# Kernel tuning notes

Hardware: AMD Instinct MI355X
Metric: run time of the kernel (lower is better)

The kernel has to match this reference:

```python
import jax, jax.numpy as jnp
import numpy as np
import math

B, T, C = 2, 2048, 1024
N_HEADS = 16  # config.head_size in the original (actually number of heads)
HEAD_DIM = C // N_HEADS


def setup_inputs() -> dict:
    key = jax.random.key(0)
    k1, k2, k3 = jax.random.split(key, 3)
    s = 1.0 / math.sqrt(C)
    return {
        "x": jax.random.normal(k1, (B, T, C), dtype=jnp.float32),
        "W_attn": jax.random.normal(k2, (C, 3 * C), dtype=jnp.float32) * s,
        "b_attn": jnp.zeros((3 * C,), dtype=jnp.float32),
        "W_proj": jax.random.normal(k3, (C, C), dtype=jnp.float32) * s,
        "b_proj": jnp.zeros((C,), dtype=jnp.float32),
    }


def reference(x, W_attn, b_attn, W_proj, b_proj):
    Bsz, Tlen, Cdim = x.shape
    qkv = x @ W_attn + b_attn                      # [B,T,3C]
    q, k, v = jnp.split(qkv, 3, axis=-1)
    # [B,T,C] -> [B,H,T,D]
    def to_heads(t):
        return t.reshape(Bsz, Tlen, N_HEADS, HEAD_DIM).transpose(0, 2, 1, 3)
    q, k, v = to_heads(q), to_heads(k), to_heads(v)
    # NOTE: original multiplies by sqrt(head_dim) (faithful to source, not 1/sqrt)
    scale = jnp.asarray(math.sqrt(HEAD_DIM), dtype=x.dtype)
    att = jnp.einsum("bhqd,bhkd->bhqk", q, k) * scale
    causal = jnp.tril(jnp.ones((Tlen, Tlen), dtype=bool))
    att = jnp.where(causal[None, None, :, :], att, jnp.asarray(-jnp.inf, x.dtype))
    att = jax.nn.softmax(att, axis=-1)
    # dropout layers are identity in eval mode
    y = jnp.einsum("bhqk,bhkd->bhqd", att, v)
    y = y.transpose(0, 2, 1, 3).reshape(Bsz, Tlen, Cdim)
    return y @ W_proj + b_proj
```

## Files before the change

kernel.cpp:

```cpp
#include <hip/hip_runtime.h>
#include <hip/hip_bf16.h>


#define B_  2
#define T_  2048
#define C_  1024
#define H_  16
#define D_  64
#define M_  (B_ * T_)
#define N3_ (3 * C_)

typedef __attribute__((ext_vector_type(8))) short s16x8;
typedef __attribute__((ext_vector_type(4))) short s16x4;
typedef __attribute__((ext_vector_type(4))) float f32x4;

typedef const __attribute__((address_space(1))) unsigned int gu32_t;
typedef __attribute__((address_space(3))) unsigned int lu32_t;

__device__ __forceinline__ void gload_lds16(const short* g, short* l) {
    __builtin_amdgcn_global_load_lds((gu32_t*)g, (lu32_t*)l, 16, 0, 0);
}

__device__ __forceinline__ float b2f(unsigned short u) {
    return __uint_as_float(((unsigned)u) << 16);
}
__device__ __forceinline__ unsigned short f2b(float f) {
    unsigned u = __float_as_uint(f);
    return (unsigned short)((u + 0x7FFFu + ((u >> 16) & 1u)) >> 16);
}
__device__ __forceinline__ float fexp2(float x) {
#if __has_builtin(__builtin_amdgcn_exp2f)
    return __builtin_amdgcn_exp2f(x);
#else
    return exp2f(x);
#endif
}

__global__ __launch_bounds__(256) void cvt_split(
    const float* __restrict__ in, short* __restrict__ oh, short* __restrict__ ol, int n)
{
    int i = (blockIdx.x * 256 + threadIdx.x) * 8;
    if (i >= n) return;
    float4 a = *(const float4*)&in[i];
    float4 b = *(const float4*)&in[i + 4];
    float v[8] = {a.x, a.y, a.z, a.w, b.x, b.y, b.z, b.w};
    s16x8 h, l;
    #pragma unroll
    for (int j = 0; j < 8; j++) {
        unsigned short hb = f2b(v[j]);
        h[j] = (short)hb;
        l[j] = (short)f2b(v[j] - b2f(hb));
    }
    *(s16x8*)&oh[i] = h;
    *(s16x8*)&ol[i] = l;
}

__global__ __launch_bounds__(256) void cvtT_split(
    const float* __restrict__ in, short* __restrict__ oh, short* __restrict__ ol,
    int R, int Cn)
{
    __shared__ short th[64][80];
    __shared__ short tl[64][80];
    const int tid = threadIdx.x;
    const int k0 = blockIdx.y * 64;
    const int n0 = blockIdx.x * 64;
    {
        int rl = tid >> 4, cl = (tid & 15) * 4;
        #pragma unroll
        for (int i = 0; i < 4; i++) {
            int kr = rl + i * 16;
            float4 v4 = *(const float4*)&in[(size_t)(k0 + kr) * Cn + n0 + cl];
            float v[4] = {v4.x, v4.y, v4.z, v4.w};
            #pragma unroll
            for (int j = 0; j < 4; j++) {
                unsigned short hb = f2b(v[j]);
                th[cl + j][kr] = (short)hb;
                tl[cl + j][kr] = (short)f2b(v[j] - b2f(hb));
            }
        }
    }
    __syncthreads();
    {
        int ro = tid >> 2, co = (tid & 3) * 16;
        *(s16x8*)&oh[(size_t)(n0 + ro) * R + k0 + co]     = *(s16x8*)&th[ro][co];
        *(s16x8*)&oh[(size_t)(n0 + ro) * R + k0 + co + 8] = *(s16x8*)&th[ro][co + 8];
        *(s16x8*)&ol[(size_t)(n0 + ro) * R + k0 + co]     = *(s16x8*)&tl[ro][co];
        *(s16x8*)&ol[(size_t)(n0 + ro) * R + k0 + co + 8] = *(s16x8*)&tl[ro][co + 8];
    }
}

__global__ __launch_bounds__(256) void cvtT_bf16(
    const float* __restrict__ in, short* __restrict__ out, int R, int Cn)
{
    __shared__ short t[64][80];
    const int tid = threadIdx.x;
    const int k0 = blockIdx.y * 64;
    const int n0 = blockIdx.x * 64;
    {
        int rl = tid >> 4, cl = (tid & 15) * 4;
        #pragma unroll
        for (int i = 0; i < 4; i++) {
            int kr = rl + i * 16;
            float4 v = *(const float4*)&in[(size_t)(k0 + kr) * Cn + n0 + cl];
            t[cl + 0][kr] = (short)f2b(v.x);
            t[cl + 1][kr] = (short)f2b(v.y);
            t[cl + 2][kr] = (short)f2b(v.z);
            t[cl + 3][kr] = (short)f2b(v.w);
        }
    }
    __syncthreads();
    {
        int ro = tid >> 2, co = (tid & 3) * 16;
        *(s16x8*)&out[(size_t)(n0 + ro) * R + k0 + co]     = *(s16x8*)&t[ro][co];
        *(s16x8*)&out[(size_t)(n0 + ro) * R + k0 + co + 8] = *(s16x8*)&t[ro][co + 8];
    }
}

__global__ __launch_bounds__(256) void qkv_qk(
    const short* __restrict__ Ah, const short* __restrict__ Al,
    const short* __restrict__ BTh, const short* __restrict__ BTl,
    const float* __restrict__ bias,
    short* __restrict__ Qh, short* __restrict__ Ql,
    short* __restrict__ Kh, short* __restrict__ Kl)
{
    __shared__ short Ash[128 * 32], Asl[128 * 32];
    __shared__ short Bsh[128 * 32], Bsl[128 * 32];

    const int tid  = threadIdx.x;
    const int wave = tid >> 6, lane = tid & 63;
    const int wm = wave >> 1, wn = wave & 1;
    const int lm = lane & 15, lq = lane >> 4;
    const int m0 = blockIdx.y * 128, n0 = blockIdx.x * 128;
    const int gr = (lane >> 2);
    const int gc = (lane & 3) * 8;

    f32x4 acc[4][4] = {};

    for (int k0 = 0; k0 < C_; k0 += 32) {
        __syncthreads();
        #pragma unroll
        for (int j = 0; j < 2; j++) {
            int s = wave * 2 + j;
            int row = s * 16 + gr;
            size_t ga = (size_t)(m0 + row) * C_ + k0 + gc;
            size_t gb = (size_t)(n0 + row) * C_ + k0 + gc;
            gload_lds16(&Ah[ga],  &Ash[s * 512]);
            gload_lds16(&Al[ga],  &Asl[s * 512]);
            gload_lds16(&BTh[gb], &Bsh[s * 512]);
            gload_lds16(&BTl[gb], &Bsl[s * 512]);
        }
        __syncthreads();

        s16x8 ah[4], al[4], bh[4], bl[4];
        #pragma unroll
        for (int mi = 0; mi < 4; mi++) {
            int r = wm * 64 + mi * 16 + lm;
            ah[mi] = *(const s16x8*)&Ash[r * 32 + lq * 8];
            al[mi] = *(const s16x8*)&Asl[r * 32 + lq * 8];
        }
        #pragma unroll
        for (int nj = 0; nj < 4; nj++) {
            int r = wn * 64 + nj * 16 + lm;
            bh[nj] = *(const s16x8*)&Bsh[r * 32 + lq * 8];
            bl[nj] = *(const s16x8*)&Bsl[r * 32 + lq * 8];
        }
        #pragma unroll
        for (int mi = 0; mi < 4; mi++)
            #pragma unroll
            for (int nj = 0; nj < 4; nj++) {
                acc[mi][nj] = __builtin_amdgcn_mfma_f32_16x16x32_bf16(
                    ah[mi], bh[nj], acc[mi][nj], 0, 0, 0);
                acc[mi][nj] = __builtin_amdgcn_mfma_f32_16x16x32_bf16(
                    ah[mi], bl[nj], acc[mi][nj], 0, 0, 0);
                acc[mi][nj] = __builtin_amdgcn_mfma_f32_16x16x32_bf16(
                    al[mi], bh[nj], acc[mi][nj], 0, 0, 0);
            }
    }

    #pragma unroll
    for (int nj = 0; nj < 4; nj++) {
        int n = n0 + wn * 64 + nj * 16 + lm;
        float bv = bias[n];
        int isK = n >> 10;
        int c = n & (C_ - 1);
        int h = c >> 6, d = c & (D_ - 1);
        short* dh = isK ? Kh : Qh;
        short* dl = isK ? Kl : Ql;
        float scale = isK ? 1.0f : 11.541560327111708f;
        #pragma unroll
        for (int mi = 0; mi < 4; mi++) {
            #pragma unroll
            for (int r = 0; r < 4; r++) {
                int m  = m0 + wm * 64 + mi * 16 + lq * 4 + r;
                int bb = m >> 11, t = m & (T_ - 1);
                float v = (acc[mi][nj][r] + bv) * scale;
                size_t idx = (((size_t)bb * H_ + h) * T_ + t) * D_ + d;
                unsigned short hb = f2b(v);
                dh[idx] = (short)hb;
                dl[idx] = (short)f2b(v - b2f(hb));
            }
        }
    }
}

__global__ __launch_bounds__(256) void qkv_v(
    const short* __restrict__ Ah, const short* __restrict__ BTh,
    const float* __restrict__ bias, short* __restrict__ VT)
{
    __shared__ short Ash[128 * 32];
    __shared__ short Bsh[128 * 32];

    const int tid  = threadIdx.x;
    const int wave = tid >> 6, lane = tid & 63;
    const int wm = wave >> 1, wn = wave & 1;
    const int lm = lane & 15, lq = lane >> 4;
    const int m0 = blockIdx.y * 128, n0 = blockIdx.x * 128;
    const int gr = (lane >> 2);
    const int gc = (lane & 3) * 8;

    f32x4 acc[4][4] = {};

    for (int k0 = 0; k0 < C_; k0 += 32) {
        __syncthreads();
        #pragma unroll
        for (int j = 0; j < 2; j++) {
            int s = wave * 2 + j;
            int row = s * 16 + gr;
            gload_lds16(&Ah[(size_t)(m0 + row) * C_ + k0 + gc],  &Ash[s * 512]);
            gload_lds16(&BTh[(size_t)(n0 + row) * C_ + k0 + gc], &Bsh[s * 512]);
        }
        __syncthreads();

        s16x8 af[4], bfr[4];
        #pragma unroll
        for (int mi = 0; mi < 4; mi++)
            af[mi] = *(const s16x8*)&Ash[(wm * 64 + mi * 16 + lm) * 32 + lq * 8];
        #pragma unroll
        for (int nj = 0; nj < 4; nj++)
            bfr[nj] = *(const s16x8*)&Bsh[(wn * 64 + nj * 16 + lm) * 32 + lq * 8];
        #pragma unroll
        for (int mi = 0; mi < 4; mi++)
            #pragma unroll
            for (int nj = 0; nj < 4; nj++)
                acc[mi][nj] = __builtin_amdgcn_mfma_f32_16x16x32_bf16(
                    af[mi], bfr[nj], acc[mi][nj], 0, 0, 0);
    }

    #pragma unroll
    for (int nj = 0; nj < 4; nj++) {
        int n = n0 + wn * 64 + nj * 16 + lm;
        float bv = bias[n];
        int h = n >> 6, d = n & (D_ - 1);
        #pragma unroll
        for (int mi = 0; mi < 4; mi++) {
            #pragma unroll
            for (int r = 0; r < 4; r++) {
                int m  = m0 + wm * 64 + mi * 16 + lq * 4 + r;
                int bb = m >> 11, t = m & (T_ - 1);
                VT[(((size_t)bb * H_ + h) * D_ + d) * T_ + t] =
                    (short)f2b(acc[mi][nj][r] + bv);
            }
        }
    }
}

__global__ __launch_bounds__(256) void proj_mfma(
    const short* __restrict__ A, const short* __restrict__ BT,
    const float* __restrict__ bias, float* __restrict__ out)
{
    __shared__ short Ash[128 * 32];
    __shared__ short Bsh[128 * 32];

    const int tid  = threadIdx.x;
    const int wave = tid >> 6, lane = tid & 63;
    const int wm = wave >> 1, wn = wave & 1;
    const int lm = lane & 15, lq = lane >> 4;
    const int m0 = blockIdx.y * 128, n0 = blockIdx.x * 128;
    const int gr = (lane >> 2);
    const int gc = (lane & 3) * 8;

    f32x4 acc[4][4] = {};

    for (int k0 = 0; k0 < C_; k0 += 32) {
        __syncthreads();
        #pragma unroll
        for (int j = 0; j < 2; j++) {
            int s = wave * 2 + j;
            int row = s * 16 + gr;
            gload_lds16(&A[(size_t)(m0 + row) * C_ + k0 + gc],  &Ash[s * 512]);
            gload_lds16(&BT[(size_t)(n0 + row) * C_ + k0 + gc], &Bsh[s * 512]);
        }
        __syncthreads();

        s16x8 af[4], bfr[4];
        #pragma unroll
        for (int mi = 0; mi < 4; mi++)
            af[mi] = *(const s16x8*)&Ash[(wm * 64 + mi * 16 + lm) * 32 + lq * 8];
        #pragma unroll
        for (int nj = 0; nj < 4; nj++)
            bfr[nj] = *(const s16x8*)&Bsh[(wn * 64 + nj * 16 + lm) * 32 + lq * 8];
        #pragma unroll
        for (int mi = 0; mi < 4; mi++)
            #pragma unroll
            for (int nj = 0; nj < 4; nj++)
                acc[mi][nj] = __builtin_amdgcn_mfma_f32_16x16x32_bf16(
                    af[mi], bfr[nj], acc[mi][nj], 0, 0, 0);
    }

    #pragma unroll
    for (int nj = 0; nj < 4; nj++) {
        int n = n0 + wn * 64 + nj * 16 + lm;
        float bv = bias[n];
        #pragma unroll
        for (int mi = 0; mi < 4; mi++) {
            #pragma unroll
            for (int r = 0; r < 4; r++) {
                int m = m0 + wm * 64 + mi * 16 + lq * 4 + r;
                out[(size_t)m * C_ + n] = acc[mi][nj][r] + bv;
            }
        }
    }
}

__global__ __launch_bounds__(256) void attn_mfma(
    const short* __restrict__ Qh, const short* __restrict__ Ql,
    const short* __restrict__ Kh, const short* __restrict__ Kl,
    const short* __restrict__ VT, short* __restrict__ Yb)
{
    __shared__ short Ksh[64][72], Ksl[64][72];
    __shared__ short Vt [64][72];
    __shared__ short Ps [4][16][72];

    const int tid  = threadIdx.x;
    const int wave = tid >> 6, lane = tid & 63;
    const int lm   = lane & 15, quad = lane >> 4;

    const int bid = blockIdx.x;
    const int xcd = bid & 7;
    const int r_  = bid >> 3;
    const int bhl = r_ & 3;
    const int u   = r_ >> 2;
    const int g_  = u >> 3, j_ = u & 7;
    const int qt  = (g_ == 0) ? j_ : (g_ == 1) ? 15 - j_
                  : (g_ == 2) ? 16 + j_ : 31 - j_;
    const int bh  = xcd * 4 + bhl;
    const int b   = bh >> 4, h = bh & (H_ - 1);
    const int q0  = qt * 64;
    const size_t base  = (size_t)bh * T_ * D_;
    const size_t vbase = (size_t)bh * D_ * T_;

    const int src = tid >> 3;
    const int sch = (tid & 7) * 8;

    #pragma unroll
    for (int i = 0; i < 2; i++) {
        int row = i * 32 + src;
        size_t gq = base + (size_t)(q0 + row) * D_ + sch;
        *(s16x8*)&Ksh[row][sch] = *(const s16x8*)&Qh[gq];
        *(s16x8*)&Ksl[row][sch] = *(const s16x8*)&Ql[gq];
    }
    __syncthreads();
    s16x8 bqh[2], bql[2];
    #pragma unroll
    for (int kc = 0; kc < 2; kc++) {
        bqh[kc] = *(const s16x8*)&Ksh[wave * 16 + lm][kc * 32 + quad * 8];
        bql[kc] = *(const s16x8*)&Ksl[wave * 16 + lm][kc * 32 + quad * 8];
    }

    s16x8 pkh[2], pkl[2], pvt[2];
    #pragma unroll
    for (int i = 0; i < 2; i++) {
        int row = i * 32 + src;
        size_t gk = base + (size_t)row * D_ + sch;
        pkh[i] = *(const s16x8*)&Kh[gk];
        pkl[i] = *(const s16x8*)&Kl[gk];
        pvt[i] = *(const s16x8*)&VT[vbase + (size_t)row * T_ + sch];
    }

    float mrow = -INFINITY, lrow = 0.f;
    f32x4 O[4] = {};

    for (int kt = 0; kt <= qt; kt++) {
        __syncthreads();
        #pragma unroll
        for (int i = 0; i < 2; i++) {
            int row = i * 32 + src;
            *(s16x8*)&Ksh[row][sch] = pkh[i];
            *(s16x8*)&Ksl[row][sch] = pkl[i];
            *(s16x8*)&Vt [row][sch] = pvt[i];
        }
        if (kt < qt) {
            #pragma unroll
            for (int i = 0; i < 2; i++) {
                int row = i * 32 + src;
                size_t gk = base + (size_t)((kt + 1) * 64 + row) * D_ + sch;
                pkh[i] = *(const s16x8*)&Kh[gk];
                pkl[i] = *(const s16x8*)&Kl[gk];
                pvt[i] = *(const s16x8*)&VT[vbase + (size_t)row * T_ + (kt + 1) * 64 + sch];
            }
        }
        __syncthreads();

        f32x4 S[4] = {};
        #pragma unroll
        for (int t = 0; t < 4; t++) {
            #pragma unroll
            for (int kc = 0; kc < 2; kc++) {
                s16x8 kh8 = *(const s16x8*)&Ksh[t * 16 + lm][kc * 32 + quad * 8];
                s16x8 kl8 = *(const s16x8*)&Ksl[t * 16 + lm][kc * 32 + quad * 8];
                S[t] = __builtin_amdgcn_mfma_f32_16x16x32_bf16(kh8, bqh[kc], S[t], 0, 0, 0);
                S[t] = __builtin_amdgcn_mfma_f32_16x16x32_bf16(kl8, bqh[kc], S[t], 0, 0, 0);
                S[t] = __builtin_amdgcn_mfma_f32_16x16x32_bf16(kh8, bql[kc], S[t], 0, 0, 0);
            }
        }

        const int qg = wave * 16 + lm;
        if (kt == qt) {
            #pragma unroll
            for (int t = 0; t < 4; t++)
                #pragma unroll
                for (int r = 0; r < 4; r++)
                    if ((t * 16 + quad * 4 + r) > qg) S[t][r] = -INFINITY;
        }

        float rm = -INFINITY;
        #pragma unroll
        for (int t = 0; t < 4; t++)
            #pragma unroll
            for (int r = 0; r < 4; r++) rm = fmaxf(rm, S[t][r]);
        rm = fmaxf(rm, __shfl_xor(rm, 16, 64));
        rm = fmaxf(rm, __shfl_xor(rm, 32, 64));
        float mnew  = fmaxf(mrow, rm);
        float alpha = fexp2(mrow - mnew);
        mrow = mnew;
        float rs = 0.f;
        #pragma unroll
        for (int t = 0; t < 4; t++)
            #pragma unroll
            for (int r = 0; r < 4; r++) {
                S[t][r] = fexp2(S[t][r] - mnew);
                rs += S[t][r];
            }
        rs += __shfl_xor(rs, 16, 64);
        rs += __shfl_xor(rs, 32, 64);
        lrow = lrow * alpha + rs;

        float al[4];
        #pragma unroll
        for (int r = 0; r < 4; r++) al[r] = __shfl(alpha, quad * 4 + r, 64);
        #pragma unroll
        for (int t = 0; t < 4; t++)
            #pragma unroll
            for (int r = 0; r < 4; r++) O[t][r] *= al[r];

        #pragma unroll
        for (int t = 0; t < 4; t++) {
            s16x4 p;
            #pragma unroll
            for (int r = 0; r < 4; r++)
                p[r] = (short)(__float_as_uint(S[t][r]) >> 16);
            *(s16x4*)&Ps[wave][lm][t * 16 + quad * 4] = p;
        }

        s16x8 ap[2];
        #pragma unroll
        for (int kc = 0; kc < 2; kc++)
            ap[kc] = *(const s16x8*)&Ps[wave][lm][kc * 32 + quad * 8];
        #pragma unroll
        for (int t = 0; t < 4; t++) {
            #pragma unroll
            for (int kc = 0; kc < 2; kc++) {
                s16x8 bv = *(const s16x8*)&Vt[t * 16 + lm][kc * 32 + quad * 8];
                O[t] = __builtin_amdgcn_mfma_f32_16x16x32_bf16(ap[kc], bv, O[t], 0, 0, 0);
            }
        }
    }

    float li[4];
    #pragma unroll
    for (int r = 0; r < 4; r++)
        li[r] = 1.0f / __shfl(lrow, quad * 4 + r, 64);
    #pragma unroll
    for (int t = 0; t < 4; t++)
        #pragma unroll
        for (int r = 0; r < 4; r++) {
            int q = q0 + wave * 16 + quad * 4 + r;
            int d = t * 16 + lm;
            Yb[((size_t)b * T_ + q) * C_ + h * D_ + d] =
                (short)f2b(O[t][r] * li[r]);
        }
}

extern "C" void kernel_launch(void* const* d_in, const int* in_sizes, int n_in,
                              void* d_out, int out_size, void* d_ws, size_t ws_size,
                              hipStream_t stream)
{
    const float* x      = (const float*)d_in[0];
    const float* W_attn = (const float*)d_in[1];
    const float* b_attn = (const float*)d_in[2];
    const float* W_proj = (const float*)d_in[3];
    const float* b_proj = (const float*)d_in[4];
    float* out = (float*)d_out;

    char* ws = (char*)d_ws;
    const size_t MB = 1024 * 1024;
    short* Qh   = (short*)(ws);
    short* Ql   = (short*)(ws +  8 * MB);
    short* Kh   = (short*)(ws + 16 * MB);
    short* Kl   = (short*)(ws + 24 * MB);
    short* xh   = (short*)(ws + 32 * MB);
    short* xl   = (short*)(ws + 40 * MB);
    short* WaTh = (short*)(ws + 48 * MB);
    short* WaTl = (short*)(ws + 54 * MB);
    short* WpT  = (short*)(ws + 60 * MB);
    short* VT   = (short*)(ws + 40 * MB);
    short* Yb   = (short*)(ws + 32 * MB);

    cvt_split <<<dim3(M_ * C_ / 2048), 256, 0, stream>>>(x, xh, xl, M_ * C_);
    cvtT_split<<<dim3(N3_ / 64, C_ / 64), 256, 0, stream>>>(W_attn, WaTh, WaTl, C_, N3_);
    cvtT_bf16 <<<dim3(C_ / 64, C_ / 64), 256, 0, stream>>>(W_proj, WpT, C_, C_);

    qkv_qk <<<dim3(16, 32), 256, 0, stream>>>(xh, xl, WaTh, WaTl, b_attn,
                                              Qh, Ql, Kh, Kl);
    qkv_v  <<<dim3(8, 32), 256, 0, stream>>>(xh, WaTh + (size_t)2048 * C_,
                                             b_attn + 2048, VT);
    attn_mfma<<<dim3(1024), 256, 0, stream>>>(Qh, Ql, Kh, Kl, VT, Yb);
    proj_mfma<<<dim3(8, 32), 256, 0, stream>>>(Yb, WpT, b_proj, out);
}
```

Before: 255.3 us.

## Pair mirrored query tiles per block to share K/V loads and balance causal work

Each attention block now handles two query tiles (j and 31-j), so K/V tiles staged in LDS serve both, and every block does the same amount of causal work. The grid is halved to 512 blocks. LDS rows drop their padding and use an XOR swizzle instead to avoid bank conflicts. Online softmax gains a lazy rescale that skips correcting O and l while the running max grows by no more than 8, plus tree reductions. The costs are higher register pressure from two sets of accumulators, fewer blocks in flight, and P values that can grow up to 2^8 before the skipped rescale, which affects bf16 rounding.

```diff
diff --git a/kernel.cpp b/kernel.cpp
--- a/kernel.cpp
+++ b/kernel.cpp
@@ -16,6 +16,8 @@
 
 typedef const __attribute__((address_space(1))) unsigned int gu32_t;
 typedef __attribute__((address_space(3))) unsigned int lu32_t;
+
+#define MFMA16(a, b, c) __builtin_amdgcn_mfma_f32_16x16x32_bf16(a, b, c, 0, 0, 0)
 
 __device__ __forceinline__ void gload_lds16(const short* g, short* l) {
     __builtin_amdgcn_global_load_lds((gu32_t*)g, (lu32_t*)l, 16, 0, 0);
@@ -322,18 +324,66 @@
     }
 }
 
-__global__ __launch_bounds__(256) void attn_mfma(
+__device__ __forceinline__ void online_sm(
+    f32x4 S[4], float& mrow, float& lrow, f32x4 O[4], int quad)
+{
+    float v[16];
+    #pragma unroll
+    for (int t = 0; t < 4; t++)
+        #pragma unroll
+        for (int r = 0; r < 4; r++) v[t * 4 + r] = S[t][r];
+    #pragma unroll
+    for (int s = 8; s; s >>= 1)
+        #pragma unroll
+        for (int i = 0; i < s; i++) v[i] = fmaxf(v[i], v[i + s]);
+    float rm = v[0];
+    rm = fmaxf(rm, __shfl_xor(rm, 16, 64));
+    rm = fmaxf(rm, __shfl_xor(rm, 32, 64));
+    if (!__all(rm - mrow <= 8.f)) {
+        float mnew  = fmaxf(mrow, rm);
+        float alpha = fexp2(mrow - mnew);
+        mrow = mnew;
+        lrow *= alpha;
+        float al[4];
+        #pragma unroll
+        for (int r = 0; r < 4; r++) al[r] = __shfl(alpha, quad * 4 + r, 64);
+        #pragma unroll
+        for (int t = 0; t < 4; t++)
+            #pragma unroll
+            for (int r = 0; r < 4; r++) O[t][r] *= al[r];
+    }
+    float sv[16];
+    #pragma unroll
+    for (int t = 0; t < 4; t++)
+        #pragma unroll
+        for (int r = 0; r < 4; r++) {
+            float p = fexp2(S[t][r] - mrow);
+            S[t][r] = p;
+            sv[t * 4 + r] = p;
+        }
+    #pragma unroll
+    for (int s = 8; s; s >>= 1)
+        #pragma unroll
+        for (int i = 0; i < s; i++) sv[i] += sv[i + s];
+    float rs = sv[0];
+    rs += __shfl_xor(rs, 16, 64);
+    rs += __shfl_xor(rs, 32, 64);
+    lrow += rs;
+}
+
+__global__ __launch_bounds__(256, 2) void attn_mfma(
     const short* __restrict__ Qh, const short* __restrict__ Ql,
     const short* __restrict__ Kh, const short* __restrict__ Kl,
     const short* __restrict__ VT, short* __restrict__ Yb)
 {
-    __shared__ short Ksh[64][72], Ksl[64][72];
-    __shared__ short Vt [64][72];
-    __shared__ short Ps [4][16][72];
+    __shared__ short Ksh[64][64], Ksl[64][64];
+    __shared__ short Vt [64][64];
+    __shared__ short Ps [4][2][16][64];
 
     const int tid  = threadIdx.x;
     const int wave = tid >> 6, lane = tid & 63;
     const int lm   = lane & 15, quad = lane >> 4;
+    const int swz  = (lm & 7) << 3;
 
     const int bid = blockIdx.x;
     const int xcd = bid & 7;
@@ -341,30 +391,27 @@
     const int bhl = r_ & 3;
     const int u   = r_ >> 2;
     const int g_  = u >> 3, j_ = u & 7;
-    const int qt  = (g_ == 0) ? j_ : (g_ == 1) ? 15 - j_
-                  : (g_ == 2) ? 16 + j_ : 31 - j_;
+    const int j   = g_ ? (15 - j_) : j_;
     const int bh  = xcd * 4 + bhl;
     const int b   = bh >> 4, h = bh & (H_ - 1);
-    const int q0  = qt * 64;
+    const int qtA = j, qtB = 31 - j;
+    const int q0A = qtA * 64, q0B = qtB * 64;
     const size_t base  = (size_t)bh * T_ * D_;
     const size_t vbase = (size_t)bh * D_ * T_;
 
     const int src = tid >> 3;
     const int sch = (tid & 7) * 8;
-
-    #pragma unroll
-    for (int i = 0; i < 2; i++) {
-        int row = i * 32 + src;
-        size_t gq = base + (size_t)(q0 + row) * D_ + sch;
-        *(s16x8*)&Ksh[row][sch] = *(const s16x8*)&Qh[gq];
-        *(s16x8*)&Ksl[row][sch] = *(const s16x8*)&Ql[gq];
-    }
-    __syncthreads();
-    s16x8 bqh[2], bql[2];
+    const int wsw = sch ^ ((src & 7) << 3);
+
+    s16x8 bqhA[2], bqlA[2], bqhB[2], bqlB[2];
     #pragma unroll
     for (int kc = 0; kc < 2; kc++) {
-        bqh[kc] = *(const s16x8*)&Ksh[wave * 16 + lm][kc * 32 + quad * 8];
-        bql[kc] = *(const s16x8*)&Ksl[wave * 16 + lm][kc * 32 + quad * 8];
+        size_t ga = base + (size_t)(q0A + wave * 16 + lm) * D_ + kc * 32 + quad * 8;
+        size_t gb = base + (size_t)(q0B + wave * 16 + lm) * D_ + kc * 32 + quad * 8;
+        bqhA[kc] = *(const s16x8*)&Qh[ga];
+        bqlA[kc] = *(const s16x8*)&Ql[ga];
+        bqhB[kc] = *(const s16x8*)&Qh[gb];
+        bqlB[kc] = *(const s16x8*)&Ql[gb];
     }
 
     s16x8 pkh[2], pkl[2], pvt[2];
@@ -377,19 +424,20 @@
         pvt[i] = *(const s16x8*)&VT[vbase + (size_t)row * T_ + sch];
     }
 
-    float mrow = -INFINITY, lrow = 0.f;
-    f32x4 O[4] = {};
-
-    for (int kt = 0; kt <= qt; kt++) {
+    float mA = -INFINITY, lA = 0.f;
+    float mB = -INFINITY, lB = 0.f;
+    f32x4 OA[4] = {}, OB[4] = {};
+
+    for (int kt = 0; kt <= qtB; kt++) {
         __syncthreads();
         #pragma unroll
         for (int i = 0; i < 2; i++) {
             int row = i * 32 + src;
-            *(s16x8*)&Ksh[row][sch] = pkh[i];
-            *(s16x8*)&Ksl[row][sch] = pkl[i];
-            *(s16x8*)&Vt [row][sch] = pvt[i];
-        }
-        if (kt < qt) {
+            *(s16x8*)&Ksh[row][wsw] = pkh[i];
+            *(s16x8*)&Ksl[row][wsw] = pkl[i];
+            *(s16x8*)&Vt [row][wsw] = pvt[i];
+        }
+        if (kt < qtB) {
             #pragma unroll
             for (int i = 0; i < 2; i++) {
                 int row = i * 32 + src;
@@ -401,93 +449,118 @@
         }
         __syncthreads();
 
-        f32x4 S[4] = {};
-        #pragma unroll
-        for (int t = 0; t < 4; t++) {
-            #pragma unroll
-            for (int kc = 0; kc < 2; kc++) {
-                s16x8 kh8 = *(const s16x8*)&Ksh[t * 16 + lm][kc * 32 + quad * 8];
-                s16x8 kl8 = *(const s16x8*)&Ksl[t * 16 + lm][kc * 32 + quad * 8];
-                S[t] = __builtin_amdgcn_mfma_f32_16x16x32_bf16(kh8, bqh[kc], S[t], 0, 0, 0);
-                S[t] = __builtin_amdgcn_mfma_f32_16x16x32_bf16(kl8, bqh[kc], S[t], 0, 0, 0);
-                S[t] = __builtin_amdgcn_mfma_f32_16x16x32_bf16(kh8, bql[kc], S[t], 0, 0, 0);
-            }
-        }
-
-        const int qg = wave * 16 + lm;
-        if (kt == qt) {
+        const bool doA = (kt <= qtA);
+        const int  qg  = wave * 16 + lm;
+
+        f32x4 SB[4] = {}, SA[4] = {};
+        if (doA) {
+            #pragma unroll
+            for (int t = 0; t < 4; t++)
+                #pragma unroll
+                for (int kc = 0; kc < 2; kc++) {
+                    s16x8 kh8 = *(const s16x8*)&Ksh[t * 16 + lm][(kc * 32 + quad * 8) ^ swz];
+                    s16x8 kl8 = *(const s16x8*)&Ksl[t * 16 + lm][(kc * 32 + quad * 8) ^ swz];
+                    SB[t] = MFMA16(kh8, bqhB[kc], SB[t]);
+                    SB[t] = MFMA16(kl8, bqhB[kc], SB[t]);
+                    SB[t] = MFMA16(kh8, bqlB[kc], SB[t]);
+                    SA[t] = MFMA16(kh8, bqhA[kc], SA[t]);
+                    SA[t] = MFMA16(kl8, bqhA[kc], SA[t]);
+                    SA[t] = MFMA16(kh8, bqlA[kc], SA[t]);
+                }
+        } else {
+            #pragma unroll
+            for (int t = 0; t < 4; t++)
+                #pragma unroll
+                for (int kc = 0; kc < 2; kc++) {
+                    s16x8 kh8 = *(const s16x8*)&Ksh[t * 16 + lm][(kc * 32 + quad * 8) ^ swz];
+                    s16x8 kl8 = *(const s16x8*)&Ksl[t * 16 + lm][(kc * 32 + quad * 8) ^ swz];
+                    SB[t] = MFMA16(kh8, bqhB[kc], SB[t]);
+                    SB[t] = MFMA16(kl8, bqhB[kc], SB[t]);
+                    SB[t] = MFMA16(kh8, bqlB[kc], SB[t]);
+                }
+        }
+
+        if (kt == qtB) {
             #pragma unroll
             for (int t = 0; t < 4; t++)
                 #pragma unroll
                 for (int r = 0; r < 4; r++)
-                    if ((t * 16 + quad * 4 + r) > qg) S[t][r] = -INFINITY;
-        }
-
-        float rm = -INFINITY;
-        #pragma unroll
-        for (int t = 0; t < 4; t++)
-            #pragma unroll
-            for (int r = 0; r < 4; r++) rm = fmaxf(rm, S[t][r]);
-        rm = fmaxf(rm, __shfl_xor(rm, 16, 64));
-        rm = fmaxf(rm, __shfl_xor(rm, 32, 64));
-        float mnew  = fmaxf(mrow, rm);
-        float alpha = fexp2(mrow - mnew);
-        mrow = mnew;
-        float rs = 0.f;
-        #pragma unroll
-        for (int t = 0; t < 4; t++)
-            #pragma unroll
-            for (int r = 0; r < 4; r++) {
-                S[t][r] = fexp2(S[t][r] - mnew);
-                rs += S[t][r];
-            }
-        rs += __shfl_xor(rs, 16, 64);
-        rs += __shfl_xor(rs, 32, 64);
-        lrow = lrow * alpha + rs;
-
-        float al[4];
-        #pragma unroll
-        for (int r = 0; r < 4; r++) al[r] = __shfl(alpha, quad * 4 + r, 64);
-        #pragma unroll
-        for (int t = 0; t < 4; t++)
-            #pragma unroll
-            for (int r = 0; r < 4; r++) O[t][r] *= al[r];
+                    if ((t * 16 + quad * 4 + r) > qg) SB[t][r] = -INFINITY;
+        }
+        if (kt == qtA) {
+            #pragma unroll
+            for (int t = 0; t < 4; t++)
+                #pragma unroll
+                for (int r = 0; r < 4; r++)
+                    if ((t * 16 + quad * 4 + r) > qg) SA[t][r] = -INFINITY;
+        }
+
+        online_sm(SB, mB, lB, OB, quad);
+        if (doA) online_sm(SA, mA, lA, OA, quad);
 
         #pragma unroll
         for (int t = 0; t < 4; t++) {
             s16x4 p;
             #pragma unroll
             for (int r = 0; r < 4; r++)
-                p[r] = (short)(__float_as_uint(S[t][r]) >> 16);
-            *(s16x4*)&Ps[wave][lm][t * 16 + quad * 4] = p;
-        }
-
-        s16x8 ap[2];
+                p[r] = (short)(__float_as_uint(SB[t][r]) >> 16);
+            *(s16x4*)&Ps[wave][0][lm][(t * 16 + quad * 4) ^ swz] = p;
+        }
+        if (doA) {
+            #pragma unroll
+            for (int t = 0; t < 4; t++) {
+                s16x4 p;
+                #pragma unroll
+                for (int r = 0; r < 4; r++)
+                    p[r] = (short)(__float_as_uint(SA[t][r]) >> 16);
+                *(s16x4*)&Ps[wave][1][lm][(t * 16 + quad * 4) ^ swz] = p;
+            }
+        }
+
+        s16x8 apB[2], apA[2];
         #pragma unroll
         for (int kc = 0; kc < 2; kc++)
-            ap[kc] = *(const s16x8*)&Ps[wave][lm][kc * 32 + quad * 8];
-        #pragma unroll
-        for (int t = 0; t < 4; t++) {
-            #pragma unroll
-            for (int kc = 0; kc < 2; kc++) {
-                s16x8 bv = *(const s16x8*)&Vt[t * 16 + lm][kc * 32 + quad * 8];
-                O[t] = __builtin_amdgcn_mfma_f32_16x16x32_bf16(ap[kc], bv, O[t], 0, 0, 0);
-            }
-        }
-    }
-
-    float li[4];
-    #pragma unroll
-    for (int r = 0; r < 4; r++)
-        li[r] = 1.0f / __shfl(lrow, quad * 4 + r, 64);
+            apB[kc] = *(const s16x8*)&Ps[wave][0][lm][(kc * 32 + quad * 8) ^ swz];
+        if (doA) {
+            #pragma unroll
+            for (int kc = 0; kc < 2; kc++)
+                apA[kc] = *(const s16x8*)&Ps[wave][1][lm][(kc * 32 + quad * 8) ^ swz];
+            #pragma unroll
+            for (int t = 0; t < 4; t++)
+                #pragma unroll
+                for (int kc = 0; kc < 2; kc++) {
+                    s16x8 bv = *(const s16x8*)&Vt[t * 16 + lm][(kc * 32 + quad * 8) ^ swz];
+                    OB[t] = MFMA16(apB[kc], bv, OB[t]);
+                    OA[t] = MFMA16(apA[kc], bv, OA[t]);
+                }
+        } else {
+            #pragma unroll
+            for (int t = 0; t < 4; t++)
+                #pragma unroll
+                for (int kc = 0; kc < 2; kc++) {
+                    s16x8 bv = *(const s16x8*)&Vt[t * 16 + lm][(kc * 32 + quad * 8) ^ swz];
+                    OB[t] = MFMA16(apB[kc], bv, OB[t]);
+                }
+        }
+    }
+
+    float liA[4], liB[4];
+    #pragma unroll
+    for (int r = 0; r < 4; r++) {
+        liA[r] = 1.0f / __shfl(lA, quad * 4 + r, 64);
+        liB[r] = 1.0f / __shfl(lB, quad * 4 + r, 64);
+    }
     #pragma unroll
     for (int t = 0; t < 4; t++)
         #pragma unroll
         for (int r = 0; r < 4; r++) {
-            int q = q0 + wave * 16 + quad * 4 + r;
-            int d = t * 16 + lm;
-            Yb[((size_t)b * T_ + q) * C_ + h * D_ + d] =
-                (short)f2b(O[t][r] * li[r]);
+            int d  = t * 16 + lm;
+            int qa = q0A + wave * 16 + quad * 4 + r;
+            int qb = q0B + wave * 16 + quad * 4 + r;
+            Yb[((size_t)b * T_ + qa) * C_ + h * D_ + d] =
+                (short)f2b(OA[t][r] * liA[r]);
+            Yb[((size_t)b * T_ + qb) * C_ + h * D_ + d] =
+                (short)f2b(OB[t][r] * liB[r]);
         }
 }
 
@@ -524,6 +597,6 @@
                                               Qh, Ql, Kh, Kl);
     qkv_v  <<<dim3(8, 32), 256, 0, stream>>>(xh, WaTh + (size_t)2048 * C_,
                                              b_attn + 2048, VT);
-    attn_mfma<<<dim3(1024), 256, 0, stream>>>(Qh, Ql, Kh, Kl, VT, Yb);
+    attn_mfma<<<dim3(512), 256, 0, stream>>>(Qh, Ql, Kh, Kl, VT, Yb);
     proj_mfma<<<dim3(8, 32), 256, 0, stream>>>(Yb, WpT, b_proj, out);
 }
```

Result: faster. 247.7 us (-3.0%).
